# Kernel optimization log

Measured on AMD Instinct MI355X. Metric: run time of the kernel, lower is better.

## Reference

```python
import jax, jax.numpy as jnp
import numpy as np

B, P, D_ENC, D_DEC, D_ATT, E, V, T = 64, 144, 1792, 512, 512, 300, 32000, 30
LN_EPS = 1e-5


def _ln(x, g, b):
    m = x.mean(-1, keepdims=True)
    v = jnp.var(x, axis=-1, keepdims=True)
    return (x - m) * jax.lax.rsqrt(v + LN_EPS) * g + b


def setup_inputs() -> dict:
    key = jax.random.key(0)
    ks = iter(jax.random.split(key, 40))
    r = lambda shape, s=0.02: (jax.random.normal(next(ks), shape, jnp.float32) * s)
    inp = {}
    inp['features'] = jax.random.normal(next(ks), (B, P, D_ENC), jnp.float32)
    inp['captions'] = jax.random.randint(next(ks), (B, T), 0, V, jnp.int32)
    inp['emb_table'] = r((V, E), 0.05)
    # attention params
    inp['ln_q_g'] = jnp.ones((D_DEC,), jnp.float32)
    inp['ln_q_b'] = jnp.zeros((D_DEC,), jnp.float32)
    inp['ln_kv_g'] = jnp.ones((D_ENC,), jnp.float32)
    inp['ln_kv_b'] = jnp.zeros((D_ENC,), jnp.float32)
    inp['Wq'] = r((D_DEC, D_ATT)); inp['bq'] = jnp.zeros((D_ATT,), jnp.float32)
    inp['Wk'] = r((D_ENC, D_ATT)); inp['bk'] = jnp.zeros((D_ATT,), jnp.float32)
    inp['Wbeta'] = r((D_DEC, 1)); inp['bbeta'] = jnp.zeros((1,), jnp.float32)
    # LSTM gate params, packed as [in_dim, 4*H] in gate order (i, f, o, g).
    # Context fed to the LSTM is the attention output of dim encoder_dim (V = normalized features).
    inp['Wh'] = r((D_DEC, 4 * D_DEC))
    inp['Wu'] = r((E, 4 * D_DEC))
    inp['Wa'] = r((D_ENC, 4 * D_DEC))
    inp['b_gates'] = jnp.zeros((4 * D_DEC,), jnp.float32)  # linear biases + extra b_* params combined
    # output head
    inp['W_Lh'] = r((D_DEC, E)); inp['b_Lh'] = jnp.zeros((E,), jnp.float32)
    inp['W_Lz'] = r((D_ENC, E)); inp['b_Lz'] = jnp.zeros((E,), jnp.float32)
    inp['W_Lo'] = r((E, V)); inp['b_Lo'] = jnp.zeros((V,), jnp.float32)
    # init state
    inp['W_ih'] = r((D_ENC, D_DEC)); inp['b_ih'] = jnp.zeros((D_DEC,), jnp.float32)
    inp['W_ic'] = r((D_ENC, D_DEC)); inp['b_ic'] = jnp.zeros((D_DEC,), jnp.float32)
    return inp


def reference(features, captions, emb_table, ln_q_g, ln_q_b, ln_kv_g, ln_kv_b,
              Wq, bq, Wk, bk, Wbeta, bbeta, Wh, Wu, Wa, b_gates,
              W_Lh, b_Lh, W_Lz, b_Lz, W_Lo, b_Lo, W_ih, b_ih, W_ic, b_ic):
    scale = jnp.sqrt(jnp.asarray(Wq.shape[1], jnp.float32))
    # features are constant across timesteps -> hoist ln_kv and K projection
    feats_n = _ln(features, ln_kv_g, ln_kv_b)          # [B,P,Denc]
    K = feats_n @ Wk + bk                               # [B,P,A]
    mean_a = features.mean(axis=1)                      # [B,Denc]
    h0 = mean_a @ W_ih + b_ih
    c0 = mean_a @ W_ic + b_ic
    embs = emb_table[captions]                          # [B,T,E] (dropout = identity in eval)
    xs = jnp.swapaxes(embs[:, :-1], 0, 1)               # [T-1,B,E], embedding at step t is word t-1

    def step(carry, emb_t):
        h, c = carry
        hq = _ln(h, ln_q_g, ln_q_b)                     # [B,H]
        Q = hq @ Wq + bq                                # [B,A]
        scores = jnp.einsum('ba,bpa->bp', Q, K) / scale
        alpha = jax.nn.softmax(scores, axis=-1)         # [B,P]
        context = jnp.einsum('bp,bpd->bd', alpha, feats_n)  # [B,Denc]
        beta = jax.nn.sigmoid(hq @ Wbeta + bbeta)       # [B,1]
        z = beta * context
        gates = h @ Wh + emb_t @ Wu + z @ Wa + b_gates  # [B,4H]
        i_t, f_t, o_t, g_t = jnp.split(gates, 4, axis=-1)
        c_new = jax.nn.sigmoid(f_t) * c + jax.nn.sigmoid(i_t) * jnp.tanh(g_t)
        h_new = jax.nn.sigmoid(o_t) * jnp.tanh(c_new)
        out_o = emb_t + (h_new @ W_Lh + b_Lh) + (z @ W_Lz + b_Lz)
        logits = out_o @ W_Lo + b_Lo                    # [B,V]
        return (h_new, c_new), (logits, alpha)

    _, (logits, alphas) = jax.lax.scan(step, (h0, c0), xs)
    # step t=0 stays zero, as in the original torch loop (range(1, seq_len))
    predictions = jnp.concatenate(
        [jnp.zeros((1,) + logits.shape[1:], logits.dtype), logits], axis=0).swapaxes(0, 1)
    alphas_out = jnp.concatenate(
        [jnp.zeros((1,) + alphas.shape[1:], alphas.dtype), alphas], axis=0).swapaxes(0, 1)
    return predictions, alphas_out
```

## Files before the change

### kernel.cpp

```cpp
#include <hip/hip_runtime.h>
#include <hip/hip_bf16.h>


#define NB 64
#define NP 144
#define DE 1792
#define DD 512
#define DA 512
#define EM 300
#define NV 32000
#define NTT 30
#define NS 29
#define G4 2048
#define KP 320
#define KG1 2304
#define LN_EPS 1e-5f
#define RSCALE 0.044194173824159216f
#define KSPL 12

typedef __attribute__((ext_vector_type(8))) short short8;
typedef __attribute__((ext_vector_type(4))) float f32x4;
typedef __attribute__((ext_vector_type(8))) unsigned short ushort8v;

__device__ __forceinline__ float bf2f(unsigned short u){
  union { unsigned int i; float f; } w; w.i = ((unsigned int)u) << 16; return w.f;
}
__device__ __forceinline__ unsigned short f2bf(float f){
  union { float f; unsigned int i; } u; u.f = f;
  unsigned int r = u.i + 0x7FFFu + ((u.i >> 16) & 1u);
  return (unsigned short)(r >> 16);
}
__device__ __forceinline__ float sigm(float x){ return 1.f/(1.f + __expf(-x)); }

__device__ __forceinline__ float wave_reduce_sum(float v){
  #pragma unroll
  for (int o = 32; o >= 1; o >>= 1) v += __shfl_xor(v, o);
  return v;
}
__device__ __forceinline__ float wave_reduce_max(float v){
  #pragma unroll
  for (int o = 32; o >= 1; o >>= 1) v = fmaxf(v, __shfl_xor(v, o));
  return v;
}
__device__ __forceinline__ float block_sum256(float v, float* sbuf){
  v = wave_reduce_sum(v);
  const int lane = threadIdx.x & 63, wid = threadIdx.x >> 6;
  if (lane == 0) sbuf[wid] = v;
  __syncthreads();
  const float r = sbuf[0] + sbuf[1] + sbuf[2] + sbuf[3];
  __syncthreads();
  return r;
}
__device__ __forceinline__ float block_sum512(float v, float* sbuf8){
  v = wave_reduce_sum(v);
  const int lane = threadIdx.x & 63, wid = threadIdx.x >> 6;
  if (lane == 0) sbuf8[wid] = v;
  __syncthreads();
  float r = 0.f;
  #pragma unroll
  for (int i = 0; i < 8; ++i) r += sbuf8[i];
  __syncthreads();
  return r;
}

__device__ __forceinline__ void stage_tile(const unsigned short* __restrict__ src,
    int row_stride, int k0, char* lds){
  const int tid = threadIdx.x;
  #pragma unroll
  for (int c = 0; c < 2; ++c){
    const int o = tid + c*256;
    const int m = o >> 3, ks8 = o & 7;
    const ushort8v v = *(const ushort8v*)&src[(size_t)m*row_stride + k0 + ks8*8];
    *(ushort8v*)&lds[m*128 + ((ks8 ^ (m&7))<<4)] = v;
  }
}
// ... 37 lines not shown
    }
    __syncthreads();
    #pragma unroll
    for (int ks = 0; ks < 2; ++ks){
      const int slot = ks*4 + (lane>>4);
      short8 af[8];
      #pragma unroll
      for (int fm = 0; fm < 8; ++fm){
        const int m = fm*16 + (lane&15);
        af[fm] = *(const short8*)&Alds[m*128 + ((slot ^ (m&7))<<4)];
      }
      #pragma unroll
      for (int fn = 0; fn < 4; ++fn){
        const int n = w*64 + fn*16 + (lane&15);
        const short8 bfv = *(const short8*)&Blds[n*128 + ((slot ^ (n&7))<<4)];
        #pragma unroll
        for (int fm = 0; fm < 8; ++fm)
          acc[fm][fn] = __builtin_amdgcn_mfma_f32_16x16x32_bf16(af[fm], bfv, acc[fm][fn], 0, 0, 0);
      }
    }
  }
}

__global__ __launch_bounds__(256) void k_zero(float* __restrict__ pred,
                                              float* __restrict__ alph){
  const int idx = blockIdx.x * 256 + threadIdx.x;
  {
    const int b = idx / NV, v = idx - b * NV;
    pred[(size_t)b * NTT * NV + v] = 0.f;
  }
  if (idx < NB * NP){
    const int b = idx / NP, p = idx - b * NP;
    alph[(size_t)b * NTT * NP + p] = 0.f;
  }
}

__global__ __launch_bounds__(256) void k_ln_feats(const float* __restrict__ feats,
    const float* __restrict__ g, const float* __restrict__ bb,
    unsigned short* __restrict__ out){
  __shared__ float sbuf[4];
  const int row = blockIdx.x;
  const float* x = feats + (size_t)row * DE;
  float v[7]; float s = 0.f;
  #pragma unroll
  for (int i = 0; i < 7; ++i){ v[i] = x[i*256 + threadIdx.x]; s += v[i]; }
  const float mean = block_sum256(s, sbuf) * (1.f/DE);
  float q = 0.f;
  #pragma unroll
  for (int i = 0; i < 7; ++i){ const float d = v[i] - mean; q += d*d; }
  const float var = block_sum256(q, sbuf) * (1.f/DE);
  const float rinv = rsqrtf(var + LN_EPS);
  #pragma unroll
  for (int i = 0; i < 7; ++i){
    const int idx = i*256 + threadIdx.x;
    out[(size_t)row*DE + idx] = f2bf((v[i]-mean)*rinv*g[idx] + bb[idx]);
  }
}

__global__ __launch_bounds__(256) void k_mean(const float* __restrict__ feats,
                                              float* __restrict__ mean_a){
  const int idx = blockIdx.x * 256 + threadIdx.x;
  const int b = idx / DE, d = idx - b * DE;
  const float* p = feats + (size_t)b * NP * DE + d;
  float s = 0.f;
  for (int pp = 0; pp < NP; ++pp) s += p[(size_t)pp * DE];
  mean_a[idx] = s * (1.f/NP);
}

__global__ __launch_bounds__(256) void k_cvt_all(
    const float* __restrict__ W_Lo, const float* __restrict__ Wh,
    const float* __restrict__ Wu,  const float* __restrict__ Wa,
    const float* __restrict__ Wk,  const float* __restrict__ W_Lh,
    const float* __restrict__ W_Lz,
    unsigned short* __restrict__ wlo_t, unsigned short* __restrict__ whT,
    unsigned short* __restrict__ wut,   unsigned short* __restrict__ wat,
    unsigned short* __restrict__ WkT,   unsigned short* __restrict__ WLt){
  __shared__ float t[64][65];
  int lb = blockIdx.x;
  if (lb >= 4036){
    lb -= 4036;
    const int e0 = (lb % 5)*64, k0 = (lb / 5)*64;
    for (int i = threadIdx.x; i < 4096; i += 256){
      const int k = i>>6, e2 = i&63;
      const int kg = k0 + k, e = e0 + e2;
      float v = 0.f;
      if (e < EM) v = (kg < DD) ? W_Lh[(size_t)kg*EM + e] : W_Lz[(size_t)(kg-DD)*EM + e];
      t[k][e2] = v;
    }
    __syncthreads();
    for (int i = threadIdx.x; i < 4096; i += 256){
      const int e2 = i>>6, k = i&63;
      WLt[(size_t)(e0+e2)*KG1 + k0+k] = f2bf(t[k][e2]);
    }
    return;
  }
  const float* src; unsigned short* dst; int K, N, KPad, nx;
  if      (lb < 2500){             src=W_Lo; dst=wlo_t; K=EM; N=NV; KPad=KP; nx=500; }
  else if (lb < 2756){ lb -= 2500; src=Wh;   dst=whT;   K=DD; N=G4; KPad=DD; nx=32; }
  else if (lb < 2916){ lb -= 2756; src=Wu;   dst=wut;   K=EM; N=G4; KPad=KP; nx=32; }
  else if (lb < 3812){ lb -= 2916; src=Wa;   dst=wat;   K=DE; N=G4; KPad=DE; nx=32; }
  else               { lb -= 3812; src=Wk;   dst=WkT;   K=DE; N=DD; KPad=DE; nx=8;  }
  const int n0 = (lb % nx)*64, k0 = (lb / nx)*64;
  for (int i = threadIdx.x; i < 4096; i += 256){
    const int k = i>>6, n = i&63;
    t[k][n] = (k0 + k < K) ? src[(size_t)(k0+k)*N + n0+n] : 0.f;
  }
  __syncthreads();
  for (int i = threadIdx.x; i < 4096; i += 256){
    const int n = i>>6, k = i&63;
    dst[(size_t)(n0+n)*KPad + k0+k] = f2bf(t[k][n]);
  }
}

__global__ __launch_bounds__(256) void k_wg(const float* __restrict__ Wq,
    const float* __restrict__ g, unsigned short* __restrict__ Wg){
  const int idx = blockIdx.x*256 + threadIdx.x;
  const int k = idx >> 9;
  Wg[idx] = f2bf(g[k]*Wq[idx]);
}

__global__ __launch_bounds__(512) void k_prep(const float* __restrict__ Wq,
    const float* __restrict__ bk, const float* __restrict__ g,
    const float* __restrict__ bln, const float* __restrict__ bq,
    const float* __restrict__ Wbeta, const float* __restrict__ bbeta,
    float* __restrict__ vq, float* __restrict__ u_,
    float* __restrict__ voff, float* __restrict__ gw,
    float* __restrict__ cscal){
  __shared__ float sbuf8[8];
  const int a = threadIdx.x;
  {
    const float* row = Wq + (size_t)a*DA;
    float acc = 0.f;
    for (int j = 0; j < DA; ++j) acc = fmaf(row[j], bk[j], acc);
    vq[a] = acc;
  }
  float uu = 0.f, vv = 0.f;
  for (int k = 0; k < DD; ++k){
    const float wv = Wq[(size_t)k*DA + a];
    uu = fmaf(g[k],   wv, uu);
    vv = fmaf(bln[k], wv, vv);
  }
  const float vo = vv + bq[a];
  u_[a]   = uu;
  voff[a] = vo;
  gw[a]   = g[a]*Wbeta[a];
  const float c1 = block_sum512(g[a]*Wbeta[a], sbuf8);
  const float c2 = block_sum512(bln[a]*Wbeta[a], sbuf8);
  const float c3 = block_sum512(uu*bk[a], sbuf8);
  const float c4 = block_sum512(vo*bk[a], sbuf8);
  if (a == 0){ cscal[0]=c1; cscal[1]=c2+bbeta[0]; cscal[2]=c3; cscal[3]=c4; }
}

__global__ __launch_bounds__(256) void k_KF(const unsigned short* __restrict__ fb,
    const unsigned short* __restrict__ WkT, unsigned short* __restrict__ KF){
  __shared__ char Alds[128*128];
  __shared__ char Blds[256*128];
  const int bid = blockIdx.x;
  const int wgid = (bid & 7)*18 + (bid >> 3);
  const int nt = wgid & 1, mt = wgid >> 1;
  const int tid = threadIdx.x, w = tid>>6, lane = tid&63;
  f32x4 acc[8][4];
  #pragma unroll
  for (int i = 0; i < 8; ++i)
    #pragma unroll
    for (int j = 0; j < 4; ++j) acc[i][j] = (f32x4)(0.f);
  gemm_big<28>(fb, WkT, DE, DE, Alds, Blds, mt, nt, acc);
  const int ncol0 = nt*256 + w*64 + (lane&15);
  #pragma unroll
  for (int fm = 0; fm < 8; ++fm)
    #pragma unroll
    for (int r = 0; r < 4; ++r){
      const int row = mt*128 + fm*16 + (lane>>4)*4 + r;
      #pragma unroll
      for (int fn = 0; fn < 4; ++fn)
        KF[(size_t)row*DD + ncol0 + fn*16] = f2bf(acc[fm][fn][r]);
    }
}

__global__ __launch_bounds__(256) void k_QG2(const unsigned short* __restrict__ KF,
    const unsigned short* __restrict__ Wg, const float* __restrict__ g_,
    const float* __restrict__ vq, unsigned short* __restrict__ G2){
  __shared__ char Alds[128*128];
  __shared__ char Blds[256*128];
  const int bid = blockIdx.x;
  const int wgid = (bid & 7)*18 + (bid >> 3);
  const int nt = wgid & 1, mt = wgid >> 1;
  const int tid = threadIdx.x, w = tid>>6, lane = tid&63;
  f32x4 acc[8][4];
  #pragma unroll
  for (int i = 0; i < 8; ++i)
    #pragma unroll
    for (int j = 0; j < 4; ++j) acc[i][j] = (f32x4)(0.f);
  gemm_big<8>(KF, Wg, DD, DD, Alds, Blds, mt, nt, acc);
  const int ncol0 = nt*256 + w*64 + (lane&15);
  float addv[4];
  #pragma unroll
  for (int fn = 0; fn < 4; ++fn){
    const int q = ncol0 + fn*16;
    addv[fn] = g_[q]*vq[q];
  }
  #pragma unroll
  for (int fm = 0; fm < 8; ++fm)
    #pragma unroll
    for (int r = 0; r < 4; ++r){
      const int row = mt*128 + fm*16 + (lane>>4)*4 + r;
      #pragma unroll
      for (int fn = 0; fn < 4; ++fn)
        G2[(size_t)row*DD + ncol0 + fn*16] = f2bf(acc[fm][fn][r] + addv[fn]);
    }
}

__global__ __launch_bounds__(512) void k_sc12(const unsigned short* __restrict__ KF,
    const float* __restrict__ u_, const float* __restrict__ voff,
    const float* __restrict__ cscal, float2* __restrict__ sc12){
  const int w = threadIdx.x>>6, lane = threadIdx.x&63;
  const int row = blockIdx.x*8 + w;
  const unsigned short* kf = KF + (size_t)row*DD + lane*8;
  float s1 = 0.f, s2 = 0.f;
  #pragma unroll
  for (int j = 0; j < 8; ++j){
    const float kv = bf2f(kf[j]);
    s1 = fmaf(u_[lane*8 + j],   kv, s1);
    s2 = fmaf(voff[lane*8 + j], kv, s2);
  }
  s1 = wave_reduce_sum(s1);
  s2 = wave_reduce_sum(s2);
  if (lane == 0){
    float2 o; o.x = s1 + cscal[2]; o.y = s2 + cscal[3];
    sc12[row] = o;
  }
}

__global__ __launch_bounds__(256) void k_init_g(const float* __restrict__ mean_a,
    const float* __restrict__ W_ih, const float* __restrict__ b_ih,
    const float* __restrict__ W_ic, const float* __restrict__ b_ic,
    float* __restrict__ hbuf, unsigned short* __restrict__ hstbf,
    float* __restrict__ cb0){
  __shared__ float la[64*68];
  __shared__ float lb[64*68];
  const int which = blockIdx.y;
  const float* W    = which ? W_ic : W_ih;
  const float* bias = which ? b_ic : b_ih;
  float* out = which ? cb0 : hbuf;
  unsigned short* outbf = which ? nullptr : hstbf;
  const int j0 = blockIdx.x*64;
  const int tid = threadIdx.x, tr = tid&15, tn = tid>>4;
  float acc[16] = {0.f};
  for (int a0 = 0; a0 < DE; a0 += 64){
    __syncthreads();
    for (int i = tid; i < 4096; i += 256){
      const int b = i>>6, k = i&63;
      la[k*68 + b] = mean_a[(size_t)b*DE + a0+k];
    }
    for (int i = tid; i < 4096; i += 256){
      const int k = i>>6, j = i&63;
      lb[k*68 + j] = W[(size_t)(a0+k)*DD + j0+j];
    }
    __syncthreads();
    for (int k = 0; k < 64; ++k){
      float av[4], bv[4];
      #pragma unroll
      for (int ii = 0; ii < 4; ++ii) av[ii] = la[k*68 + tr*4+ii];
      #pragma unroll
      for (int jj = 0; jj < 4; ++jj) bv[jj] = lb[k*68 + tn*4+jj];
      #pragma unroll
      for (int ii = 0; ii < 4; ++ii)
        #pragma unroll
        for (int jj = 0; jj < 4; ++jj)
          acc[ii*4+jj] = fmaf(av[ii], bv[jj], acc[ii*4+jj]);
    }
  }
  #pragma unroll
  for (int ii = 0; ii < 4; ++ii)
    #pragma unroll
    for (int jj = 0; jj < 4; ++jj){
      const size_t idx = (size_t)(tr*4+ii)*DD + j0 + tn*4+jj;
      const float val = acc[ii*4+jj] + bias[j0 + tn*4+jj];
      out[idx] = val;
      if (outbf) outbf[idx] = f2bf(val);
    }
}

__global__ __launch_bounds__(256) void k_EU(const float* __restrict__ emb_table,
    const int* __restrict__ captions, const unsigned short* __restrict__ wut,
    float* __restrict__ eu){
  __shared__ char Alds[8192];
  __shared__ char Blds[8192];
  __shared__ int capL[64];
  const int jt = blockIdx.x, s = blockIdx.y;
  const int tid = threadIdx.x, w = tid>>6, lane = tid&63;
  if (tid < 64) capL[tid] = captions[tid*NTT + s];
  f32x4 acc[4];
  #pragma unroll
  for (int i = 0; i < 4; ++i) acc[i] = (f32x4)(0.f);
  for (int kt = 0; kt < 5; ++kt){
    __syncthreads();
    #pragma unroll
    for (int c = 0; c < 2; ++c){
      const int o = tid + c*256;
      const int m = o>>3, ks8 = o&7;
      const int e0 = kt*64 + ks8*8;
      const float* er = emb_table + (size_t)capL[m]*EM;
      ushort8v v;
      #pragma unroll
      for (int jj = 0; jj < 8; ++jj)
        v[jj] = (e0 + jj < EM) ? f2bf(er[e0 + jj]) : (unsigned short)0;
      *(ushort8v*)&Alds[m*128 + ((ks8 ^ (m&7))<<4)] = v;
    }
    stage_tile(wut + (size_t)jt*64*KP, KP, kt*64, Blds);
    __syncthreads();
    mma64(Alds, Blds, w, lane, acc);
  }
  const int j = jt*64 + w*16 + (lane&15);
  #pragma unroll
  for (int fm = 0; fm < 4; ++fm)
    #pragma unroll
    for (int r = 0; r < 4; ++r){
      const int b = fm*16 + (lane>>4)*4 + r;
      eu[((size_t)s*NB + b)*G4 + j] = acc[fm][r];
    }
}

__global__ __launch_bounds__(512) void k_A(
    const unsigned short* __restrict__ gp, const float* __restrict__ eu,
    const float* __restrict__ b_gates, const float* __restrict__ cin,
    float* __restrict__ cout, unsigned short* __restrict__ hst,
    const unsigned short* __restrict__ G2, const float2* __restrict__ sc12,
    const unsigned short* __restrict__ fb, const float* __restrict__ gw,
    const float* __restrict__ cscal, const int s, const int do_att,
    float* __restrict__ alph, unsigned short* __restrict__ zbf){
  __shared__ alignas(16) unsigned short hL[DD];
  __shared__ float sc[NP];
  __shared__ float al[NP];
  __shared__ float sredA[8*4];
  __shared__ float sbufM[8];
  __shared__ float sbufS[8];
  int sl, b;
  if (gridDim.x == 1){ sl = 0; b = blockIdx.y; }
  else {
    const int lin = blockIdx.x + 2*blockIdx.y;
    const int xcd = lin & 7, i = lin >> 3;
    b = xcd*8 + (i & 7);
    sl = i >> 3;
// ... 142 lines not shown
      const int o = tid + c2*256;
      const int m = o>>3, ks8 = o&7;
      const int col = (m>>4)*DD + jt*16 + (m&15);
      const unsigned short* src = (k0 < DD)
          ? whT + (size_t)col*DD + k0
          : wat + (size_t)col*DE + (k0 - DD);
      const ushort8v v = *(const ushort8v*)&src[ks8*8];
      *(ushort8v*)&Blds[m*128 + ((ks8 ^ (m&7))<<4)] = v;
    }
    __syncthreads();
    mma64(Alds, Blds, w, lane, acc);
  }
  const int jcol = jt*16 + (lane&15);
  unsigned short* gps = gp + (size_t)ks*NB*G4;
  #pragma unroll
  for (int fm = 0; fm < 4; ++fm)
    #pragma unroll
    for (int r = 0; r < 4; ++r){
      const int b = fm*16 + (lane>>4)*4 + r;
      gps[(size_t)b*G4 + w*DD + jcol] = f2bf(acc[fm][r]);
    }
}

__global__ __launch_bounds__(256) void k_G1m(const unsigned short* __restrict__ hstbf,
    const unsigned short* __restrict__ zbf, const unsigned short* __restrict__ WLt,
    float* __restrict__ g1p){
  __shared__ char Alds[128*128];
  __shared__ char Blds[256*128];
  const int mt = blockIdx.x, nt = blockIdx.y, ks6 = blockIdx.z;
  const int tid = threadIdx.x, w = tid>>6, lane = tid&63;
  f32x4 acc[8][4];
  #pragma unroll
  for (int i = 0; i < 8; ++i)
    #pragma unroll
    for (int j = 0; j < 4; ++j) acc[i][j] = (f32x4)(0.f);
  for (int kt = 0; kt < 6; ++kt){
    const int k0 = ks6*384 + kt*64;
    __syncthreads();
    #pragma unroll
    for (int c2 = 0; c2 < 4; ++c2){
      const int o16 = tid + c2*256;
      const int m = o16>>3, ks8 = o16&7;
      const int r = mt*128 + m;
      ushort8v v;
      if (r < NS*NB){
        const int sS = r >> 6, bb = r & 63;
        const unsigned short* srcp = (k0 < DD)
            ? hstbf + ((size_t)(sS+1)*NB + bb)*DD + k0
            : zbf + ((size_t)sS*NB + bb)*DE + (k0 - DD);
        v = *(const ushort8v*)&srcp[ks8*8];
      } else {
        #pragma unroll
        for (int j = 0; j < 8; ++j) v[j] = 0;
      }
      *(ushort8v*)&Alds[m*128 + ((ks8 ^ (m&7))<<4)] = v;
    }
    #pragma unroll
    for (int c2 = 0; c2 < 8; ++c2){
      const int o16 = tid + c2*256;
      const int n = o16>>3, ks8 = o16&7;
// ... 3 lines not shown
      *(ushort8v*)&Blds[n*128 + ((ks8 ^ (n&7))<<4)] = v;
    }
    __syncthreads();
    #pragma unroll
    for (int ks = 0; ks < 2; ++ks){
      const int slot = ks*4 + (lane>>4);
      short8 af[8];
      #pragma unroll
      for (int fm = 0; fm < 8; ++fm){
        const int m = fm*16 + (lane&15);
        af[fm] = *(const short8*)&Alds[m*128 + ((slot ^ (m&7))<<4)];
      }
      #pragma unroll
      for (int fn = 0; fn < 4; ++fn){
        const int n = w*64 + fn*16 + (lane&15);
        const short8 bfv = *(const short8*)&Blds[n*128 + ((slot ^ (n&7))<<4)];
        #pragma unroll
        for (int fm = 0; fm < 8; ++fm)
          acc[fm][fn] = __builtin_amdgcn_mfma_f32_16x16x32_bf16(af[fm], bfv, acc[fm][fn], 0, 0, 0);
      }
    }
  }
  const int ncol0 = nt*256 + w*64 + (lane&15);
  float* dst = g1p + (size_t)ks6*NS*NB*KP;
  #pragma unroll
  for (int fm = 0; fm < 8; ++fm){
    #pragma unroll
    for (int r = 0; r < 4; ++r){
      const int row = mt*128 + fm*16 + (lane>>4)*4 + r;
      if (row < NS*NB){
        #pragma unroll
        for (int fn = 0; fn < 4; ++fn){
          const int e = ncol0 + fn*16;
          if (e < KP) dst[(size_t)row*KP + e] = acc[fm][fn][r];
        }
      }
    }
  }
}

__global__ __launch_bounds__(256) void k_G1red(const float* __restrict__ g1p,
    const float* __restrict__ b_Lh, const float* __restrict__ b_Lz,
    const float* __restrict__ emb_table, const int* __restrict__ captions,
    unsigned short* __restrict__ outo){
  const int idx = blockIdx.x*256 + threadIdx.x;
  const int row = idx / KP, e = idx - row*KP;
  const int s = row >> 6, b = row & 63;
  float v = 0.f;
  #pragma unroll
  for (int ks6 = 0; ks6 < 6; ++ks6) v += g1p[(size_t)ks6*NS*NB*KP + idx];
  if (e < EM){
    const int cap = captions[b*NTT + s];
    v += b_Lh[e] + b_Lz[e] + emb_table[(size_t)cap*EM + e];
  } else v = 0.f;
  outo[idx] = f2bf(v);
}

__global__ __launch_bounds__(256) void k_G2(const unsigned short* __restrict__ Abf,
    const unsigned short* __restrict__ Bt, const float* __restrict__ b_Lo,
    float* __restrict__ pred){
  __shared__ char Alds[128*128];
  __shared__ char Blds[256*128];
  const int bid = blockIdx.x;
  const int xcd = bid & 7, idx8 = bid >> 3;
  const int wgid = (xcd < 3 ? xcd*235 : 705 + (xcd-3)*234) + idx8;
  const int nt = wgid / 15, mt = wgid - nt*15;
  const int tid = threadIdx.x, w = tid>>6, lane = tid&63;
  f32x4 acc[8][4];
  #pragma unroll
  for (int i = 0; i < 8; ++i)
    #pragma unroll
    for (int j = 0; j < 4; ++j)
      acc[i][j] = (f32x4)(0.f);
  gemm_big<5>(Abf, Bt, KP, KP, Alds, Blds, mt, nt, acc);
  const int ncol0 = nt*256 + w*64 + (lane&15);
  #pragma unroll
  for (int fm = 0; fm < 8; ++fm){
    #pragma unroll
// ... 54 lines not shown
  unsigned short* whT      = (unsigned short*)alloc((size_t)G4*DD * 2);
  unsigned short* wut      = (unsigned short*)alloc((size_t)G4*KP * 2);
  unsigned short* wat      = (unsigned short*)alloc((size_t)G4*DE * 2);
  unsigned short* WkT      = (unsigned short*)alloc((size_t)DD*DE * 2);
  unsigned short* WLt      = (unsigned short*)alloc((size_t)KP*KG1 * 2);
  unsigned short* Wg       = (unsigned short*)alloc((size_t)DD*DD * 2);
  unsigned short* KFbf     = (unsigned short*)alloc((size_t)NB*NP*DD * 2);
  unsigned short* G2bf     = (unsigned short*)alloc((size_t)NB*NP*DD * 2);
  float2* sc12  = (float2*)alloc((size_t)NB*NP * 8);
  float* vq     = (float*)alloc((size_t)DD * 4);
  float* u_     = (float*)alloc((size_t)DD * 4);
  float* voff   = (float*)alloc((size_t)DD * 4);
  float* gw     = (float*)alloc((size_t)DD * 4);
  float* cscal  = (float*)alloc(16);
  float* mean_a = (float*)alloc((size_t)NB*DE * 4);
  float* hbuf   = (float*)alloc((size_t)NB*DD * 4);
  float* cb0    = (float*)alloc((size_t)NB*DD * 4);
  float* cb1    = (float*)alloc((size_t)NB*DD * 4);
  unsigned short* hstbf = (unsigned short*)alloc((size_t)(NS+1)*NB*DD * 2);
  unsigned short* zbf   = (unsigned short*)alloc((size_t)NS*NB*DE * 2);
  unsigned short* outo  = (unsigned short*)alloc((size_t)1920*KP * 2);
  unsigned short* gp    = (unsigned short*)alloc((size_t)KSPL*NB*G4 * 2);
  float* eu_all = (float*)alloc((size_t)NS*NB*G4 * 4);
  float* g1p    = (float*)alloc((size_t)6*NS*NB*KP * 4);
  float* cb[2] = { cb0, cb1 };

  k_zero<<<dim3((NB*NV)/256), dim3(256), 0, stream>>>(pred, alph);
  k_ln_feats<<<dim3(NB*NP), dim3(256), 0, stream>>>(features, ln_kv_g, ln_kv_b, feats_bf);
  k_mean<<<dim3((NB*DE)/256), dim3(256), 0, stream>>>(features, mean_a);
  k_cvt_all<<<dim3(4216), dim3(256), 0, stream>>>(W_Lo, Wh, Wu, Wa, Wk, W_Lh, W_Lz,
      wlo_t, whT, wut, wat, WkT, WLt);
  k_wg<<<dim3((DD*DD)/256), dim3(256), 0, stream>>>(Wq, ln_q_g, Wg);
  k_prep<<<dim3(1), dim3(512), 0, stream>>>(Wq, bk, ln_q_g, ln_q_b, bq, Wbeta,
      bbeta, vq, u_, voff, gw, cscal);
  k_KF<<<dim3(144), dim3(256), 0, stream>>>(feats_bf, WkT, KFbf);
  k_QG2<<<dim3(144), dim3(256), 0, stream>>>(KFbf, Wg, ln_q_g, vq, G2bf);
  k_sc12<<<dim3(NB*NP/8), dim3(512), 0, stream>>>(KFbf, u_, voff, cscal, sc12);
  k_init_g<<<dim3(DD/64, 2), dim3(256), 0, stream>>>(mean_a, W_ih, b_ih, W_ic, b_ic,
      hbuf, hstbf, cb0);
  k_EU<<<dim3(G4/64, NS), dim3(256), 0, stream>>>(emb_table, captions, wut, eu_all);

  for (int s = 0; s < NS; ++s){
    k_A<<<dim3(2, NB), dim3(512), 0, stream>>>(gp, eu_all, b_gates,
        cb[(s & 1) ^ 1], cb[s & 1], hstbf, G2bf, sc12, feats_bf,
        gw, cscal, s, 1, alph, zbf);
    k_B<<<dim3(32, KSPL), dim3(256), 0, stream>>>(hstbf, zbf, whT, wat, s, gp);
  }
  k_A<<<dim3(1, NB), dim3(512), 0, stream>>>(gp, eu_all, b_gates,
      cb[(NS & 1) ^ 1], cb[NS & 1], hstbf, G2bf, sc12, feats_bf,
      gw, cscal, NS, 0, alph, zbf);

  k_G1m<<<dim3(15, 2, 6), dim3(256), 0, stream>>>(hstbf, zbf, WLt, g1p);
  k_G1red<<<dim3((NS*NB*KP)/256), dim3(256), 0, stream>>>(g1p, b_Lh, b_Lz,
      emb_table, captions, outo);
  k_G2<<<dim3(1875), dim3(256), 0, stream>>>(outo, wlo_t, b_Lo, pred);
}
```

Measured before the change: 1.143 ms.

## Merge preprocessing kernels into three launches and drop split-K in G1

Eleven setup kernels (zeroing, feature LayerNorm, mean, weight transposes, Wg scaling, prep, KF, QG2, sc12, init state, EU) are packed into three block-indexed kernels, grouped by data dependency. The goal is to cut launch overhead and the idle gaps between small kernels. The G1 GEMM no longer splits K six ways with a separate reduction kernel. Each block now runs the full K loop and applies the bias, the embedding add and the bf16 store in its epilogue, which removes the fp32 partial buffer and one launch. The cost is only 30 blocks for G1, each with a K loop six times longer, so that GEMM has far less parallelism.

```diff
diff --git a/kernel.cpp b/kernel.cpp
--- a/kernel.cpp
+++ b/kernel.cpp
@@ -42,15 +42,6 @@
   for (int o = 32; o >= 1; o >>= 1) v = fmaxf(v, __shfl_xor(v, o));
   return v;
 }
-__device__ __forceinline__ float block_sum256(float v, float* sbuf){
-  v = wave_reduce_sum(v);
-  const int lane = threadIdx.x & 63, wid = threadIdx.x >> 6;
-  if (lane == 0) sbuf[wid] = v;
-  __syncthreads();
-  const float r = sbuf[0] + sbuf[1] + sbuf[2] + sbuf[3];
-  __syncthreads();
-  return r;
-}
 __device__ __forceinline__ float block_sum512(float v, float* sbuf8){
   v = wave_reduce_sum(v);
   const int lane = threadIdx.x & 63, wid = threadIdx.x >> 6;
@@ -134,303 +125,320 @@
   }
 }
 
-__global__ __launch_bounds__(256) void k_zero(float* __restrict__ pred,
-                                              float* __restrict__ alph){
-  const int idx = blockIdx.x * 256 + threadIdx.x;
-  {
-    const int b = idx / NV, v = idx - b * NV;
-    pred[(size_t)b * NTT * NV + v] = 0.f;
-  }
-  if (idx < NB * NP){
-    const int b = idx / NP, p = idx - b * NP;
-    alph[(size_t)b * NTT * NP + p] = 0.f;
-  }
-}
-
-__global__ __launch_bounds__(256) void k_ln_feats(const float* __restrict__ feats,
-    const float* __restrict__ g, const float* __restrict__ bb,
-    unsigned short* __restrict__ out){
-  __shared__ float sbuf[4];
-  const int row = blockIdx.x;
-  const float* x = feats + (size_t)row * DE;
-  float v[7]; float s = 0.f;
-  #pragma unroll
-  for (int i = 0; i < 7; ++i){ v[i] = x[i*256 + threadIdx.x]; s += v[i]; }
-  const float mean = block_sum256(s, sbuf) * (1.f/DE);
-  float q = 0.f;
-  #pragma unroll
-  for (int i = 0; i < 7; ++i){ const float d = v[i] - mean; q += d*d; }
-  const float var = block_sum256(q, sbuf) * (1.f/DE);
-  const float rinv = rsqrtf(var + LN_EPS);
-  #pragma unroll
-  for (int i = 0; i < 7; ++i){
-    const int idx = i*256 + threadIdx.x;
-    out[(size_t)row*DE + idx] = f2bf((v[i]-mean)*rinv*g[idx] + bb[idx]);
-  }
-}
-
-__global__ __launch_bounds__(256) void k_mean(const float* __restrict__ feats,
-                                              float* __restrict__ mean_a){
-  const int idx = blockIdx.x * 256 + threadIdx.x;
-  const int b = idx / DE, d = idx - b * DE;
-  const float* p = feats + (size_t)b * NP * DE + d;
-  float s = 0.f;
-  for (int pp = 0; pp < NP; ++pp) s += p[(size_t)pp * DE];
-  mean_a[idx] = s * (1.f/NP);
-}
-
-__global__ __launch_bounds__(256) void k_cvt_all(
+__global__ __launch_bounds__(512) void k_pre1(
+    const float* __restrict__ feats, const float* __restrict__ ln_kv_g,
+    const float* __restrict__ ln_kv_b,
     const float* __restrict__ W_Lo, const float* __restrict__ Wh,
     const float* __restrict__ Wu,  const float* __restrict__ Wa,
     const float* __restrict__ Wk,  const float* __restrict__ W_Lh,
     const float* __restrict__ W_Lz,
+    const float* __restrict__ Wq, const float* __restrict__ bk,
+    const float* __restrict__ g,  const float* __restrict__ bln,
+    const float* __restrict__ bq, const float* __restrict__ Wbeta,
+    const float* __restrict__ bbeta,
+    float* __restrict__ pred, float* __restrict__ alph,
+    unsigned short* __restrict__ feats_bf, float* __restrict__ mean_a,
     unsigned short* __restrict__ wlo_t, unsigned short* __restrict__ whT,
     unsigned short* __restrict__ wut,   unsigned short* __restrict__ wat,
-    unsigned short* __restrict__ WkT,   unsigned short* __restrict__ WLt){
+    unsigned short* __restrict__ WkT,   unsigned short* __restrict__ WLt,
+    unsigned short* __restrict__ Wg, float* __restrict__ vq,
+    float* __restrict__ u_, float* __restrict__ voff,
+    float* __restrict__ gw, float* __restrict__ cscal){
   __shared__ float t[64][65];
+  __shared__ float sbuf8[8];
+  const int tid = threadIdx.x;
   int lb = blockIdx.x;
-  if (lb >= 4036){
-    lb -= 4036;
-    const int e0 = (lb % 5)*64, k0 = (lb / 5)*64;
-    for (int i = threadIdx.x; i < 4096; i += 256){
-      const int k = i>>6, e2 = i&63;
-      const int kg = k0 + k, e = e0 + e2;
-      float v = 0.f;
-      if (e < EM) v = (kg < DD) ? W_Lh[(size_t)kg*EM + e] : W_Lz[(size_t)(kg-DD)*EM + e];
-      t[k][e2] = v;
+  if (lb < 4000){
+    const int idx = lb*512 + tid;
+    { const int b = idx / NV, v = idx - b*NV;
+      pred[(size_t)b*NTT*NV + v] = 0.f; }
+    if (idx < NB*NP){
+      const int b = idx / NP, p = idx - b*NP;
+      alph[(size_t)b*NTT*NP + p] = 0.f; }
+    return;
+  }
+  lb -= 4000;
+  if (lb < 9216){
+    const float* x = feats + (size_t)lb * DE;
+    float v[4]; float s = 0.f;
+    #pragma unroll
+    for (int i = 0; i < 4; ++i){
+      const int idx = i*512 + tid;
+      v[i] = (idx < DE) ? x[idx] : 0.f;
+      s += v[i];
+    }
+    const float mean = block_sum512(s, sbuf8) * (1.f/DE);
+    float q = 0.f;
+    #pragma unroll
+    for (int i = 0; i < 4; ++i){
+      const int idx = i*512 + tid;
+      if (idx < DE){ const float d = v[i] - mean; q += d*d; }
+    }
+    const float var = block_sum512(q, sbuf8) * (1.f/DE);
+    const float rinv = rsqrtf(var + LN_EPS);
+    #pragma unroll
+    for (int i = 0; i < 4; ++i){
+      const int idx = i*512 + tid;
+      if (idx < DE)
+        feats_bf[(size_t)lb*DE + idx] = f2bf((v[i]-mean)*rinv*ln_kv_g[idx] + ln_kv_b[idx]);
+    }
+    return;
+  }
+  lb -= 9216;
+  if (lb < 224){
+    const int idx = lb*512 + tid;
+    const int b = idx / DE, d = idx - b*DE;
+    const float* p = feats + (size_t)b*NP*DE + d;
+    float s = 0.f;
+    for (int pp = 0; pp < NP; ++pp) s += p[(size_t)pp*DE];
+    mean_a[idx] = s * (1.f/NP);
+    return;
+  }
+  lb -= 224;
+  if (lb < 4216){
+    if (lb >= 4036){
+      int l2 = lb - 4036;
+      const int e0 = (l2 % 5)*64, k0 = (l2 / 5)*64;
+      for (int i = tid; i < 4096; i += 512){
+        const int k = i>>6, e2 = i&63;
+        const int kg = k0 + k, e = e0 + e2;
+        float v = 0.f;
+        if (e < EM) v = (kg < DD) ? W_Lh[(size_t)kg*EM + e] : W_Lz[(size_t)(kg-DD)*EM + e];
+        t[k][e2] = v;
+      }
+      __syncthreads();
+      for (int i = tid; i < 4096; i += 512){
+        const int e2 = i>>6, k = i&63;
+        WLt[(size_t)(e0+e2)*KG1 + k0+k] = f2bf(t[k][e2]);
+      }
+      return;
+    }
+    const float* src; unsigned short* dst; int K, N, KPad, nx;
+    if      (lb < 2500){             src=W_Lo; dst=wlo_t; K=EM; N=NV; KPad=KP; nx=500; }
+    else if (lb < 2756){ lb -= 2500; src=Wh;   dst=whT;   K=DD; N=G4; KPad=DD; nx=32; }
+    else if (lb < 2916){ lb -= 2756; src=Wu;   dst=wut;   K=EM; N=G4; KPad=KP; nx=32; }
+    else if (lb < 3812){ lb -= 2916; src=Wa;   dst=wat;   K=DE; N=G4; KPad=DE; nx=32; }
+    else               { lb -= 3812; src=Wk;   dst=WkT;   K=DE; N=DD; KPad=DE; nx=8;  }
+    const int n0 = (lb % nx)*64, k0 = (lb / nx)*64;
+    for (int i = tid; i < 4096; i += 512){
+      const int k = i>>6, n = i&63;
+      t[k][n] = (k0 + k < K) ? src[(size_t)(k0+k)*N + n0+n] : 0.f;
     }
     __syncthreads();
-    for (int i = threadIdx.x; i < 4096; i += 256){
-      const int e2 = i>>6, k = i&63;
-      WLt[(size_t)(e0+e2)*KG1 + k0+k] = f2bf(t[k][e2]);
+    for (int i = tid; i < 4096; i += 512){
+      const int n = i>>6, k = i&63;
+      dst[(size_t)(n0+n)*KPad + k0+k] = f2bf(t[k][n]);
     }
     return;
   }
-  const float* src; unsigned short* dst; int K, N, KPad, nx;
-  if      (lb < 2500){             src=W_Lo; dst=wlo_t; K=EM; N=NV; KPad=KP; nx=500; }
-  else if (lb < 2756){ lb -= 2500; src=Wh;   dst=whT;   K=DD; N=G4; KPad=DD; nx=32; }
-  else if (lb < 2916){ lb -= 2756; src=Wu;   dst=wut;   K=EM; N=G4; KPad=KP; nx=32; }
-  else if (lb < 3812){ lb -= 2916; src=Wa;   dst=wat;   K=DE; N=G4; KPad=DE; nx=32; }
-  else               { lb -= 3812; src=Wk;   dst=WkT;   K=DE; N=DD; KPad=DE; nx=8;  }
-  const int n0 = (lb % nx)*64, k0 = (lb / nx)*64;
-  for (int i = threadIdx.x; i < 4096; i += 256){
-    const int k = i>>6, n = i&63;
-    t[k][n] = (k0 + k < K) ? src[(size_t)(k0+k)*N + n0+n] : 0.f;
-  }
-  __syncthreads();
-  for (int i = threadIdx.x; i < 4096; i += 256){
-    const int n = i>>6, k = i&63;
-    dst[(size_t)(n0+n)*KPad + k0+k] = f2bf(t[k][n]);
-  }
-}
-
-__global__ __launch_bounds__(256) void k_wg(const float* __restrict__ Wq,
-    const float* __restrict__ g, unsigned short* __restrict__ Wg){
-  const int idx = blockIdx.x*256 + threadIdx.x;
-  const int k = idx >> 9;
-  Wg[idx] = f2bf(g[k]*Wq[idx]);
-}
-
-__global__ __launch_bounds__(512) void k_prep(const float* __restrict__ Wq,
-    const float* __restrict__ bk, const float* __restrict__ g,
-    const float* __restrict__ bln, const float* __restrict__ bq,
-    const float* __restrict__ Wbeta, const float* __restrict__ bbeta,
-    float* __restrict__ vq, float* __restrict__ u_,
-    float* __restrict__ voff, float* __restrict__ gw,
-    float* __restrict__ cscal){
-  __shared__ float sbuf8[8];
-  const int a = threadIdx.x;
+  lb -= 4216;
+  if (lb < 512){
+    const int idx = lb*512 + tid;
+    const int k = idx >> 9;
+    Wg[idx] = f2bf(g[k]*Wq[idx]);
+    return;
+  }
   {
-    const float* row = Wq + (size_t)a*DA;
-    float acc = 0.f;
-    for (int j = 0; j < DA; ++j) acc = fmaf(row[j], bk[j], acc);
-    vq[a] = acc;
-  }
-  float uu = 0.f, vv = 0.f;
-  for (int k = 0; k < DD; ++k){
-    const float wv = Wq[(size_t)k*DA + a];
-    uu = fmaf(g[k],   wv, uu);
-    vv = fmaf(bln[k], wv, vv);
-  }
-  const float vo = vv + bq[a];
-  u_[a]   = uu;
-  voff[a] = vo;
-  gw[a]   = g[a]*Wbeta[a];
-  const float c1 = block_sum512(g[a]*Wbeta[a], sbuf8);
-  const float c2 = block_sum512(bln[a]*Wbeta[a], sbuf8);
-  const float c3 = block_sum512(uu*bk[a], sbuf8);
-  const float c4 = block_sum512(vo*bk[a], sbuf8);
-  if (a == 0){ cscal[0]=c1; cscal[1]=c2+bbeta[0]; cscal[2]=c3; cscal[3]=c4; }
-}
-
-__global__ __launch_bounds__(256) void k_KF(const unsigned short* __restrict__ fb,
-    const unsigned short* __restrict__ WkT, unsigned short* __restrict__ KF){
-  __shared__ char Alds[128*128];
-  __shared__ char Blds[256*128];
-  const int bid = blockIdx.x;
-  const int wgid = (bid & 7)*18 + (bid >> 3);
-  const int nt = wgid & 1, mt = wgid >> 1;
-  const int tid = threadIdx.x, w = tid>>6, lane = tid&63;
-  f32x4 acc[8][4];
-  #pragma unroll
-  for (int i = 0; i < 8; ++i)
-    #pragma unroll
-    for (int j = 0; j < 4; ++j) acc[i][j] = (f32x4)(0.f);
-  gemm_big<28>(fb, WkT, DE, DE, Alds, Blds, mt, nt, acc);
-  const int ncol0 = nt*256 + w*64 + (lane&15);
-  #pragma unroll
-  for (int fm = 0; fm < 8; ++fm)
-    #pragma unroll
-    for (int r = 0; r < 4; ++r){
-      const int row = mt*128 + fm*16 + (lane>>4)*4 + r;
-      #pragma unroll
-      for (int fn = 0; fn < 4; ++fn)
-        KF[(size_t)row*DD + ncol0 + fn*16] = f2bf(acc[fm][fn][r]);
-    }
-}
-
-__global__ __launch_bounds__(256) void k_QG2(const unsigned short* __restrict__ KF,
-    const unsigned short* __restrict__ Wg, const float* __restrict__ g_,
-    const float* __restrict__ vq, unsigned short* __restrict__ G2){
-  __shared__ char Alds[128*128];
-  __shared__ char Blds[256*128];
-  const int bid = blockIdx.x;
-  const int wgid = (bid & 7)*18 + (bid >> 3);
-  const int nt = wgid & 1, mt = wgid >> 1;
-  const int tid = threadIdx.x, w = tid>>6, lane = tid&63;
-  f32x4 acc[8][4];
-  #pragma unroll
-  for (int i = 0; i < 8; ++i)
-    #pragma unroll
-    for (int j = 0; j < 4; ++j) acc[i][j] = (f32x4)(0.f);
-  gemm_big<8>(KF, Wg, DD, DD, Alds, Blds, mt, nt, acc);
-  const int ncol0 = nt*256 + w*64 + (lane&15);
-  float addv[4];
-  #pragma unroll
-  for (int fn = 0; fn < 4; ++fn){
-    const int q = ncol0 + fn*16;
-    addv[fn] = g_[q]*vq[q];
-  }
-  #pragma unroll
-  for (int fm = 0; fm < 8; ++fm)
-    #pragma unroll
-    for (int r = 0; r < 4; ++r){
-      const int row = mt*128 + fm*16 + (lane>>4)*4 + r;
-      #pragma unroll
-      for (int fn = 0; fn < 4; ++fn)
-        G2[(size_t)row*DD + ncol0 + fn*16] = f2bf(acc[fm][fn][r] + addv[fn]);
-    }
-}
-
-__global__ __launch_bounds__(512) void k_sc12(const unsigned short* __restrict__ KF,
-    const float* __restrict__ u_, const float* __restrict__ voff,
-    const float* __restrict__ cscal, float2* __restrict__ sc12){
-  const int w = threadIdx.x>>6, lane = threadIdx.x&63;
-  const int row = blockIdx.x*8 + w;
-  const unsigned short* kf = KF + (size_t)row*DD + lane*8;
-  float s1 = 0.f, s2 = 0.f;
-  #pragma unroll
-  for (int j = 0; j < 8; ++j){
-    const float kv = bf2f(kf[j]);
-    s1 = fmaf(u_[lane*8 + j],   kv, s1);
-    s2 = fmaf(voff[lane*8 + j], kv, s2);
-  }
-  s1 = wave_reduce_sum(s1);
-  s2 = wave_reduce_sum(s2);
-  if (lane == 0){
-    float2 o; o.x = s1 + cscal[2]; o.y = s2 + cscal[3];
-    sc12[row] = o;
-  }
-}
-
-__global__ __launch_bounds__(256) void k_init_g(const float* __restrict__ mean_a,
+    const int a = tid;
+    {
+      const float* row = Wq + (size_t)a*DA;
+      float acc = 0.f;
+      for (int j = 0; j < DA; ++j) acc = fmaf(row[j], bk[j], acc);
+      vq[a] = acc;
+    }
+    float uu = 0.f, vv = 0.f;
+    for (int k = 0; k < DD; ++k){
+      const float wv = Wq[(size_t)k*DA + a];
+      uu = fmaf(g[k],   wv, uu);
+      vv = fmaf(bln[k], wv, vv);
+    }
+    const float vo = vv + bq[a];
+    u_[a]   = uu;
+    voff[a] = vo;
+    gw[a]   = g[a]*Wbeta[a];
+    const float c1 = block_sum512(g[a]*Wbeta[a], sbuf8);
+    const float c2 = block_sum512(bln[a]*Wbeta[a], sbuf8);
+    const float c3 = block_sum512(uu*bk[a], sbuf8);
+    const float c4 = block_sum512(vo*bk[a], sbuf8);
+    if (a == 0){ cscal[0]=c1; cscal[1]=c2+bbeta[0]; cscal[2]=c3; cscal[3]=c4; }
+  }
+}
+
+__global__ __launch_bounds__(256) void k_pre2(
+    const unsigned short* __restrict__ fb, const unsigned short* __restrict__ WkT,
+    const float* __restrict__ mean_a,
     const float* __restrict__ W_ih, const float* __restrict__ b_ih,
     const float* __restrict__ W_ic, const float* __restrict__ b_ic,
-    float* __restrict__ hbuf, unsigned short* __restrict__ hstbf,
-    float* __restrict__ cb0){
-  __shared__ float la[64*68];
-  __shared__ float lb[64*68];
-  const int which = blockIdx.y;
-  const float* W    = which ? W_ic : W_ih;
-  const float* bias = which ? b_ic : b_ih;
-  float* out = which ? cb0 : hbuf;
-  unsigned short* outbf = which ? nullptr : hstbf;
-  const int j0 = blockIdx.x*64;
-  const int tid = threadIdx.x, tr = tid&15, tn = tid>>4;
-  float acc[16] = {0.f};
-  for (int a0 = 0; a0 < DE; a0 += 64){
-    __syncthreads();
-    for (int i = tid; i < 4096; i += 256){
-      const int b = i>>6, k = i&63;
-      la[k*68 + b] = mean_a[(size_t)b*DE + a0+k];
-    }
-    for (int i = tid; i < 4096; i += 256){
-      const int k = i>>6, j = i&63;
-      lb[k*68 + j] = W[(size_t)(a0+k)*DD + j0+j];
-    }
-    __syncthreads();
-    for (int k = 0; k < 64; ++k){
-      float av[4], bv[4];
-      #pragma unroll
-      for (int ii = 0; ii < 4; ++ii) av[ii] = la[k*68 + tr*4+ii];
-      #pragma unroll
-      for (int jj = 0; jj < 4; ++jj) bv[jj] = lb[k*68 + tn*4+jj];
-      #pragma unroll
-      for (int ii = 0; ii < 4; ++ii)
-        #pragma unroll
-        for (int jj = 0; jj < 4; ++jj)
-          acc[ii*4+jj] = fmaf(av[ii], bv[jj], acc[ii*4+jj]);
-    }
-  }
-  #pragma unroll
-  for (int ii = 0; ii < 4; ++ii)
-    #pragma unroll
-    for (int jj = 0; jj < 4; ++jj){
-      const size_t idx = (size_t)(tr*4+ii)*DD + j0 + tn*4+jj;
-      const float val = acc[ii*4+jj] + bias[j0 + tn*4+jj];
-      out[idx] = val;
-      if (outbf) outbf[idx] = f2bf(val);
-    }
-}
-
-__global__ __launch_bounds__(256) void k_EU(const float* __restrict__ emb_table,
-    const int* __restrict__ captions, const unsigned short* __restrict__ wut,
+    const float* __restrict__ emb_table, const int* __restrict__ captions,
+    const unsigned short* __restrict__ wut,
+    unsigned short* __restrict__ KF, float* __restrict__ hbuf,
+    unsigned short* __restrict__ hstbf, float* __restrict__ cb0,
     float* __restrict__ eu){
-  __shared__ char Alds[8192];
-  __shared__ char Blds[8192];
-  __shared__ int capL[64];
-  const int jt = blockIdx.x, s = blockIdx.y;
+  __shared__ alignas(16) char smem[49152];
   const int tid = threadIdx.x, w = tid>>6, lane = tid&63;
-  if (tid < 64) capL[tid] = captions[tid*NTT + s];
-  f32x4 acc[4];
-  #pragma unroll
-  for (int i = 0; i < 4; ++i) acc[i] = (f32x4)(0.f);
-  for (int kt = 0; kt < 5; ++kt){
-    __syncthreads();
-    #pragma unroll
-    for (int c = 0; c < 2; ++c){
-      const int o = tid + c*256;
-      const int m = o>>3, ks8 = o&7;
-      const int e0 = kt*64 + ks8*8;
-      const float* er = emb_table + (size_t)capL[m]*EM;
-      ushort8v v;
-      #pragma unroll
-      for (int jj = 0; jj < 8; ++jj)
-        v[jj] = (e0 + jj < EM) ? f2bf(er[e0 + jj]) : (unsigned short)0;
-      *(ushort8v*)&Alds[m*128 + ((ks8 ^ (m&7))<<4)] = v;
-    }
-    stage_tile(wut + (size_t)jt*64*KP, KP, kt*64, Blds);
-    __syncthreads();
-    mma64(Alds, Blds, w, lane, acc);
-  }
-  const int j = jt*64 + w*16 + (lane&15);
-  #pragma unroll
-  for (int fm = 0; fm < 4; ++fm)
-    #pragma unroll
-    for (int r = 0; r < 4; ++r){
-      const int b = fm*16 + (lane>>4)*4 + r;
-      eu[((size_t)s*NB + b)*G4 + j] = acc[fm][r];
-    }
+  int lb = blockIdx.x;
+  if (lb < 144){
+    char* Alds = smem; char* Blds = smem + 16384;
+    const int wgid = (lb & 7)*18 + (lb >> 3);
+    const int nt = wgid & 1, mt = wgid >> 1;
+    f32x4 acc[8][4];
+    #pragma unroll
+    for (int i = 0; i < 8; ++i)
+      #pragma unroll
+      for (int j = 0; j < 4; ++j) acc[i][j] = (f32x4)(0.f);
+    gemm_big<28>(fb, WkT, DE, DE, Alds, Blds, mt, nt, acc);
+    const int ncol0 = nt*256 + w*64 + (lane&15);
+    #pragma unroll
+    for (int fm = 0; fm < 8; ++fm)
+      #pragma unroll
+      for (int r = 0; r < 4; ++r){
+        const int row = mt*128 + fm*16 + (lane>>4)*4 + r;
+        #pragma unroll
+        for (int fn = 0; fn < 4; ++fn)
+          KF[(size_t)row*DD + ncol0 + fn*16] = f2bf(acc[fm][fn][r]);
+      }
+    return;
+  }
+  lb -= 144;
+  if (lb < 16){
+    float* la = (float*)smem;
+    float* lw = (float*)smem + 64*68;
+    const int which = lb >> 3;
+    const float* W    = which ? W_ic : W_ih;
+    const float* bias = which ? b_ic : b_ih;
+    float* out = which ? cb0 : hbuf;
+    unsigned short* outbf = which ? nullptr : hstbf;
+    const int j0 = (lb & 7)*64;
+    const int tr = tid&15, tn = tid>>4;
+    float acc[16] = {0.f};
+    for (int a0 = 0; a0 < DE; a0 += 64){
+      __syncthreads();
+      for (int i = tid; i < 4096; i += 256){
+        const int b = i>>6, k = i&63;
+        la[k*68 + b] = mean_a[(size_t)b*DE + a0+k];
+      }
+      for (int i = tid; i < 4096; i += 256){
+        const int k = i>>6, j = i&63;
+        lw[k*68 + j] = W[(size_t)(a0+k)*DD + j0+j];
+      }
+      __syncthreads();
+      for (int k = 0; k < 64; ++k){
+        float av[4], bv[4];
+        #pragma unroll
+        for (int ii = 0; ii < 4; ++ii) av[ii] = la[k*68 + tr*4+ii];
+        #pragma unroll
+        for (int jj = 0; jj < 4; ++jj) bv[jj] = lw[k*68 + tn*4+jj];
+        #pragma unroll
+        for (int ii = 0; ii < 4; ++ii)
+          #pragma unroll
+          for (int jj = 0; jj < 4; ++jj)
+            acc[ii*4+jj] = fmaf(av[ii], bv[jj], acc[ii*4+jj]);
+      }
+    }
+    #pragma unroll
+    for (int ii = 0; ii < 4; ++ii)
+      #pragma unroll
+      for (int jj = 0; jj < 4; ++jj){
+        const size_t idx = (size_t)(tr*4+ii)*DD + j0 + tn*4+jj;
+        const float val = acc[ii*4+jj] + bias[j0 + tn*4+jj];
+        out[idx] = val;
+        if (outbf) outbf[idx] = f2bf(val);
+      }
+    return;
+  }
+  lb -= 16;
+  {
+    char* Alds = smem; char* Blds = smem + 8192;
+    int* capL = (int*)(smem + 16384);
+    const int jt = lb & 31, s = lb >> 5;
+    if (tid < 64) capL[tid] = captions[tid*NTT + s];
+    f32x4 acc[4];
+    #pragma unroll
+    for (int i = 0; i < 4; ++i) acc[i] = (f32x4)(0.f);
+    for (int kt = 0; kt < 5; ++kt){
+      __syncthreads();
+      #pragma unroll
+      for (int c = 0; c < 2; ++c){
+        const int o = tid + c*256;
+        const int m = o>>3, ks8 = o&7;
+        const int e0 = kt*64 + ks8*8;
+        const float* er = emb_table + (size_t)capL[m]*EM;
+        ushort8v v;
+        #pragma unroll
+        for (int jj = 0; jj < 8; ++jj)
+          v[jj] = (e0 + jj < EM) ? f2bf(er[e0 + jj]) : (unsigned short)0;
+        *(ushort8v*)&Alds[m*128 + ((ks8 ^ (m&7))<<4)] = v;
+      }
+      stage_tile(wut + (size_t)jt*64*KP, KP, kt*64, Blds);
+      __syncthreads();
+      mma64(Alds, Blds, w, lane, acc);
+    }
+    const int j = jt*64 + w*16 + (lane&15);
+    #pragma unroll
+    for (int fm = 0; fm < 4; ++fm)
+      #pragma unroll
+      for (int r = 0; r < 4; ++r){
+        const int b = fm*16 + (lane>>4)*4 + r;
+        eu[((size_t)s*NB + b)*G4 + j] = acc[fm][r];
+      }
+  }
+}
+
+__global__ __launch_bounds__(256) void k_pre3(
+    const unsigned short* __restrict__ KF, const unsigned short* __restrict__ Wg,
+    const float* __restrict__ g_, const float* __restrict__ vq,
+    const float* __restrict__ u_, const float* __restrict__ voff,
+    const float* __restrict__ cscal,
+    unsigned short* __restrict__ G2, float2* __restrict__ sc12){
+  __shared__ alignas(16) char smem[49152];
+  const int tid = threadIdx.x, w = tid>>6, lane = tid&63;
+  int lb = blockIdx.x;
+  if (lb < 144){
+    char* Alds = smem; char* Blds = smem + 16384;
+    const int wgid = (lb & 7)*18 + (lb >> 3);
+    const int nt = wgid & 1, mt = wgid >> 1;
+    f32x4 acc[8][4];
+    #pragma unroll
+    for (int i = 0; i < 8; ++i)
+      #pragma unroll
+      for (int j = 0; j < 4; ++j) acc[i][j] = (f32x4)(0.f);
+    gemm_big<8>(KF, Wg, DD, DD, Alds, Blds, mt, nt, acc);
+    const int ncol0 = nt*256 + w*64 + (lane&15);
+    float addv[4];
+    #pragma unroll
+    for (int fn = 0; fn < 4; ++fn){
+      const int q = ncol0 + fn*16;
+      addv[fn] = g_[q]*vq[q];
+    }
+    #pragma unroll
+    for (int fm = 0; fm < 8; ++fm)
+      #pragma unroll
+      for (int r = 0; r < 4; ++r){
+        const int row = mt*128 + fm*16 + (lane>>4)*4 + r;
+        #pragma unroll
+        for (int fn = 0; fn < 4; ++fn)
+          G2[(size_t)row*DD + ncol0 + fn*16] = f2bf(acc[fm][fn][r] + addv[fn]);
+      }
+    return;
+  }
+  lb -= 144;
+  {
+    const int row = lb*4 + w;
+    const unsigned short* kf = KF + (size_t)row*DD + lane*8;
+    float s1 = 0.f, s2 = 0.f;
+    #pragma unroll
+    for (int j = 0; j < 8; ++j){
+      const float kv = bf2f(kf[j]);
+      s1 = fmaf(u_[lane*8 + j],   kv, s1);
+      s2 = fmaf(voff[lane*8 + j], kv, s2);
+    }
+    s1 = wave_reduce_sum(s1);
+    s2 = wave_reduce_sum(s2);
+    if (lane == 0){
+      float2 o; o.x = s1 + cscal[2]; o.y = s2 + cscal[3];
+      sc12[row] = o;
+    }
+  }
 }
 
 __global__ __launch_bounds__(512) void k_A(
@@ -619,20 +627,22 @@
     }
 }
 
-__global__ __launch_bounds__(256) void k_G1m(const unsigned short* __restrict__ hstbf,
+__global__ __launch_bounds__(256) void k_G1(const unsigned short* __restrict__ hstbf,
     const unsigned short* __restrict__ zbf, const unsigned short* __restrict__ WLt,
-    float* __restrict__ g1p){
+    const float* __restrict__ b_Lh, const float* __restrict__ b_Lz,
+    const float* __restrict__ emb_table, const int* __restrict__ captions,
+    unsigned short* __restrict__ outo){
   __shared__ char Alds[128*128];
   __shared__ char Blds[256*128];
-  const int mt = blockIdx.x, nt = blockIdx.y, ks6 = blockIdx.z;
+  const int mt = blockIdx.x, nt = blockIdx.y;
   const int tid = threadIdx.x, w = tid>>6, lane = tid&63;
   f32x4 acc[8][4];
   #pragma unroll
   for (int i = 0; i < 8; ++i)
     #pragma unroll
     for (int j = 0; j < 4; ++j) acc[i][j] = (f32x4)(0.f);
-  for (int kt = 0; kt < 6; ++kt){
-    const int k0 = ks6*384 + kt*64;
+  for (int kt = 0; kt < 36; ++kt){
+    const int k0 = kt*64;
     __syncthreads();
     #pragma unroll
     for (int c2 = 0; c2 < 4; ++c2){
@@ -682,38 +692,27 @@
     }
   }
   const int ncol0 = nt*256 + w*64 + (lane&15);
-  float* dst = g1p + (size_t)ks6*NS*NB*KP;
   #pragma unroll
   for (int fm = 0; fm < 8; ++fm){
     #pragma unroll
     for (int r = 0; r < 4; ++r){
       const int row = mt*128 + fm*16 + (lane>>4)*4 + r;
       if (row < NS*NB){
+        const int s = row >> 6, b = row & 63;
+        const int cap = captions[b*NTT + s];
         #pragma unroll
         for (int fn = 0; fn < 4; ++fn){
           const int e = ncol0 + fn*16;
-          if (e < KP) dst[(size_t)row*KP + e] = acc[fm][fn][r];
+          if (e < KP){
+            float v = 0.f;
+            if (e < EM)
+              v = acc[fm][fn][r] + b_Lh[e] + b_Lz[e] + emb_table[(size_t)cap*EM + e];
+            outo[(size_t)row*KP + e] = f2bf(v);
+          }
         }
       }
     }
   }
-}
-
-__global__ __launch_bounds__(256) void k_G1red(const float* __restrict__ g1p,
-    const float* __restrict__ b_Lh, const float* __restrict__ b_Lz,
-    const float* __restrict__ emb_table, const int* __restrict__ captions,
-    unsigned short* __restrict__ outo){
-  const int idx = blockIdx.x*256 + threadIdx.x;
-  const int row = idx / KP, e = idx - row*KP;
-  const int s = row >> 6, b = row & 63;
-  float v = 0.f;
-  #pragma unroll
-  for (int ks6 = 0; ks6 < 6; ++ks6) v += g1p[(size_t)ks6*NS*NB*KP + idx];
-  if (e < EM){
-    const int cap = captions[b*NTT + s];
-    v += b_Lh[e] + b_Lz[e] + emb_table[(size_t)cap*EM + e];
-  } else v = 0.f;
-  outo[idx] = f2bf(v);
 }
 
 __global__ __launch_bounds__(256) void k_G2(const unsigned short* __restrict__ Abf,
@@ -814,23 +813,17 @@
   unsigned short* outo  = (unsigned short*)alloc((size_t)1920*KP * 2);
   unsigned short* gp    = (unsigned short*)alloc((size_t)KSPL*NB*G4 * 2);
   float* eu_all = (float*)alloc((size_t)NS*NB*G4 * 4);
-  float* g1p    = (float*)alloc((size_t)6*NS*NB*KP * 4);
   float* cb[2] = { cb0, cb1 };
 
-  k_zero<<<dim3((NB*NV)/256), dim3(256), 0, stream>>>(pred, alph);
-  k_ln_feats<<<dim3(NB*NP), dim3(256), 0, stream>>>(features, ln_kv_g, ln_kv_b, feats_bf);
-  k_mean<<<dim3((NB*DE)/256), dim3(256), 0, stream>>>(features, mean_a);
-  k_cvt_all<<<dim3(4216), dim3(256), 0, stream>>>(W_Lo, Wh, Wu, Wa, Wk, W_Lh, W_Lz,
-      wlo_t, whT, wut, wat, WkT, WLt);
-  k_wg<<<dim3((DD*DD)/256), dim3(256), 0, stream>>>(Wq, ln_q_g, Wg);
-  k_prep<<<dim3(1), dim3(512), 0, stream>>>(Wq, bk, ln_q_g, ln_q_b, bq, Wbeta,
-      bbeta, vq, u_, voff, gw, cscal);
-  k_KF<<<dim3(144), dim3(256), 0, stream>>>(feats_bf, WkT, KFbf);
-  k_QG2<<<dim3(144), dim3(256), 0, stream>>>(KFbf, Wg, ln_q_g, vq, G2bf);
-  k_sc12<<<dim3(NB*NP/8), dim3(512), 0, stream>>>(KFbf, u_, voff, cscal, sc12);
-  k_init_g<<<dim3(DD/64, 2), dim3(256), 0, stream>>>(mean_a, W_ih, b_ih, W_ic, b_ic,
-      hbuf, hstbf, cb0);
-  k_EU<<<dim3(G4/64, NS), dim3(256), 0, stream>>>(emb_table, captions, wut, eu_all);
+  k_pre1<<<dim3(18169), dim3(512), 0, stream>>>(features, ln_kv_g, ln_kv_b,
+      W_Lo, Wh, Wu, Wa, Wk, W_Lh, W_Lz, Wq, bk, ln_q_g, ln_q_b, bq, Wbeta,
+      bbeta, pred, alph, feats_bf, mean_a, wlo_t, whT, wut, wat, WkT, WLt,
+      Wg, vq, u_, voff, gw, cscal);
+  k_pre2<<<dim3(1088), dim3(256), 0, stream>>>(feats_bf, WkT, mean_a,
+      W_ih, b_ih, W_ic, b_ic, emb_table, captions, wut,
+      KFbf, hbuf, hstbf, cb0, eu_all);
+  k_pre3<<<dim3(2448), dim3(256), 0, stream>>>(KFbf, Wg, ln_q_g, vq,
+      u_, voff, cscal, G2bf, sc12);
 
   for (int s = 0; s < NS; ++s){
     k_A<<<dim3(2, NB), dim3(512), 0, stream>>>(gp, eu_all, b_gates,
@@ -842,8 +835,7 @@
       cb[(NS & 1) ^ 1], cb[NS & 1], hstbf, G2bf, sc12, feats_bf,
       gw, cscal, NS, 0, alph, zbf);
 
-  k_G1m<<<dim3(15, 2, 6), dim3(256), 0, stream>>>(hstbf, zbf, WLt, g1p);
-  k_G1red<<<dim3((NS*NB*KP)/256), dim3(256), 0, stream>>>(g1p, b_Lh, b_Lz,
+  k_G1<<<dim3(15, 2), dim3(256), 0, stream>>>(hstbf, zbf, WLt, b_Lh, b_Lz,
       emb_table, captions, outo);
   k_G2<<<dim3(1875), dim3(256), 0, stream>>>(outo, wlo_t, b_Lo, pred);
 }
```

Result: slower. 1.235 ms (+8.1%).
